# Kernel tuning notes

Hardware: AMD Instinct MI355X
Metric: run time of the kernel (lower is better)

Reference implementation:

```python
import jax, jax.numpy as jnp
import numpy as np

E = 8_388_608  # total edges across batched graphs
G = 4096       # num_graphs


def setup_inputs() -> dict:
    key = jax.random.key(0)
    k1, k2, k3 = jax.random.split(key, 3)
    edge_scores = jax.random.normal(k1, (E,), dtype=jnp.float32)
    # edge_batch: sorted segment ids in [0, G), as in PyG batched graphs
    edge_batch = jnp.sort(jax.random.randint(k2, (E,), 0, G)).astype(jnp.int32)
    candidate_mask = jax.random.bernoulli(k3, 0.5, (E,))
    return {
        "edge_scores": edge_scores,
        "edge_batch": edge_batch,
        "candidate_mask": candidate_mask,
        "num_graphs": G,
        "k": 32,
    }


def reference(edge_scores, edge_batch, candidate_mask, num_graphs, k):
    """Segmented top-k edge selection (GFlowNetActor._select_topk_candidate_edges).

    Faithful fixed-shape formulation: candidate edges come in as a boolean mask
    over all E edges (the rollout builds cand_edges = nonzero(candidate_mask)),
    and the kept top-k-per-graph edges go out as a boolean pruned mask (the
    rollout scatters the returned indices back into pruned_mask). Also returns
    the score values gated by the pruned mask (differentiable output).
    """
    n = edge_scores.shape[0]
    neg_inf = jnp.finfo(jnp.float32).min
    # Non-candidates get -inf so they sort to the back of each segment
    s = jnp.where(candidate_mask, edge_scores.astype(jnp.float32), neg_inf)
    # Sort by score descending, then stably by segment id -> within each
    # graph edges appear in descending-score order (same double-argsort as torch)
    order_score = jnp.argsort(-s, stable=True)
    order_seg = jnp.argsort(edge_batch[order_score], stable=True)
    perm = order_score[order_seg]          # [E] edge ids sorted by (seg asc, score desc)
    seg_sorted = edge_batch[perm]          # [E]
    # Segment starts via bincount + exclusive cumsum
    counts = jnp.bincount(seg_sorted, length=num_graphs)
    start = jnp.concatenate(
        [jnp.zeros(1, jnp.int32), jnp.cumsum(counts)[:-1].astype(jnp.int32)]
    )
    rank = jnp.arange(n, dtype=jnp.int32) - start[seg_sorted]
    keep_sorted = (rank < k) & candidate_mask[perm]
    # Scatter keep flags back to original edge order
    pruned_mask = jnp.zeros(n, dtype=bool).at[perm].set(keep_sorted)
    pruned_scores = jnp.where(pruned_mask, edge_scores, jnp.float32(0.0))
    return pruned_mask, pruned_scores
```

## Files before the change

kernel.cpp:

```cpp
#include <hip/hip_runtime.h>
#include <stdint.h>

#define G_NUM 4096
#define BLOCK 256
#define VPT   12
#define CAP   (BLOCK * VPT - 3)
#define CLS   256
#define HB    2048

typedef unsigned long long ull;

__device__ __forceinline__ unsigned int order_bits(float f) {
    unsigned int b = __float_as_uint(f);
    return (b & 0x80000000u) ? ~b : (b | 0x80000000u);
}
__device__ __forceinline__ float inv_order_bits(unsigned int ob) {
    return __uint_as_float((ob & 0x80000000u) ? (ob & 0x7FFFFFFFu) : ~ob);
}

__global__ void prep_kernel(const int* __restrict__ batch, int* __restrict__ start,
                            const unsigned int* __restrict__ mraw, int* __restrict__ flag,
                            int E) {
    if (blockIdx.x == 0 && threadIdx.x < 64) {
        int lane = threadIdx.x;
        bool allI = true, allF = true;
        for (int i = lane; i < 256; i += 64) {
            unsigned int w = mraw[i];
            if (w > 1u) allI = false;
            if (w != 0u && w != 0x3F800000u) allF = false;
        }
        allI = __all(allI);
        allF = __all(allF);
        if (lane == 0) *flag = allI ? 0 : (allF ? 1 : 2);
    }
    const int n4 = E >> 2;
    int i4 = blockIdx.x * blockDim.x + threadIdx.x;
    if (i4 >= n4) return;
    int4 b = ((const int4*)batch)[i4];
    int prev = __shfl_up(b.w, 1, 64);
    if ((threadIdx.x & 63) == 0) prev = (i4 == 0) ? -1 : batch[i4 * 4 - 1];
    const int e0 = i4 * 4;
    for (int g = prev + 1; g <= b.x; ++g) start[g] = e0;
    for (int g = b.x + 1; g <= b.y; ++g) start[g] = e0 + 1;
    for (int g = b.y + 1; g <= b.z; ++g) start[g] = e0 + 2;
    for (int g = b.z + 1; g <= b.w; ++g) start[g] = e0 + 3;
    if (i4 == n4 - 1) {
        int last = b.w, e = E & ~3;
        for (int t = 0; t < (E & 3); ++t) {
            int v = batch[e + t];
            for (int g = last + 1; g <= v; ++g) start[g] = e + t;
            last = v;
        }
        for (int g = last + 1; g <= G_NUM; ++g) start[g] = E;
    }
}

__device__ __forceinline__ void scan_select(
    unsigned int* hist, unsigned int* wtot, int kk,
    int* bsel_s, unsigned int* cgt_s, unsigned int* hsel_s, int* cnt2, int tid)
{
    unsigned int h = hist[tid];
    hist[tid] = 0u;
    unsigned int v = h;
    int lane = tid & 63, wv = tid >> 6;
    #pragma unroll
    for (int off = 1; off < 64; off <<= 1) {
        unsigned int o = __shfl_down(v, off, 64);
        if (lane + off < 64) v += o;
    }
    if (lane == 0) wtot[wv] = v;
    if (tid == 0) *cnt2 = 0;
    __syncthreads();
    unsigned int sfx = v;
    for (int w = wv + 1; w < 4; ++w) sfx += wtot[w];
    if ((unsigned)kk <= sfx && (unsigned)kk > sfx - h) {
        *bsel_s = tid; *cgt_s = sfx - h; *hsel_s = h;
    }
    __syncthreads();
}

__device__ __forceinline__ void scan_select2048(
    unsigned int* hist, unsigned int* wtot, int kk,
    int* bsel_s, unsigned int* cgt_s, unsigned int* hsel_s, int* cnt2, int tid)
{
    unsigned int h[8];
    unsigned int S = 0u;
    const int b0 = tid * 8;
    #pragma unroll
    for (int j = 0; j < 8; ++j) { h[j] = hist[b0 + j]; S += h[j]; hist[b0 + j] = 0u; }
    unsigned int v = S;
    int lane = tid & 63, wv = tid >> 6;
    #pragma unroll
    for (int off = 1; off < 64; off <<= 1) {
        unsigned int o = __shfl_down(v, off, 64);
        if (lane + off < 64) v += o;
    }
    if (lane == 0) wtot[wv] = v;
    if (tid == 0) *cnt2 = 0;
    __syncthreads();
    unsigned int sfx = v;
    for (int w = wv + 1; w < 4; ++w) sfx += wtot[w];
    unsigned int run = sfx - S;
    #pragma unroll
    for (int j = 7; j >= 0; --j) {
        unsigned int inc = run + h[j];
        if ((unsigned)kk <= inc && (unsigned)kk > run) {
            *bsel_s = b0 + j; *cgt_s = run; *hsel_s = h[j];
        }
        run = inc;
    }
    __syncthreads();
}

__global__ __launch_bounds__(BLOCK) void topk_kernel(
    const float* __restrict__ scores, const void* __restrict__ maskp,
    const int* __restrict__ start, const int* __restrict__ kp,
    const int* __restrict__ flagp, float* __restrict__ out_mask,
    float* __restrict__ out_scores, int E)
{
    __shared__ unsigned int hist[HB];
    __shared__ unsigned int wtot[4];
    __shared__ ull cls[CLS];
    __shared__ int cnt, cnt2, bsel_s, licut_s;
    __shared__ unsigned int cgt_s, hsel_s, P_s;

    const int g  = blockIdx.x;
    const int s0 = start[g];
    const int s1 = start[g + 1];
    const int len = s1 - s0;
    if (len <= 0) return;

    const int k     = *kp;
    const int mflag = *flagp;
    const int tid   = threadIdx.x;

    auto getmask = [&](int i) -> bool {
        if (mflag == 2) return ((const unsigned char*)maskp)[i] != 0;
        if (mflag == 0) return ((const int*)maskp)[i] != 0;
        return ((const float*)maskp)[i] != 0.0f;
    };

    if (k <= 0) {
        for (int i = s0 + tid; i < s1; i += BLOCK) { out_mask[i] = 0.0f; out_scores[i] = 0.0f; }
        return;
    }

    #pragma unroll
    for (int j = 0; j < HB / BLOCK; ++j) hist[tid + j * BLOCK] = 0u;
    if (tid == 0) cnt = 0;

    if (len <= CAP) {
        const int a0 = s0 & ~3;
        unsigned int key[VPT];
        unsigned int candm = 0u;

        #pragma unroll
        for (int q = 0; q < 3; ++q) {
            const int g0 = a0 + 4 * (q * BLOCK + tid);
            if (g0 >= s0 && g0 + 4 <= s1) {
                float4 f = *(const float4*)(scores + g0);
                key[4*q]   = order_bits(f.x);
                key[4*q+1] = order_bits(f.y);
                key[4*q+2] = order_bits(f.z);
                key[4*q+3] = order_bits(f.w);
                unsigned int cm4 = 0u;
                if (mflag == 2) {
                    unsigned int w = *(const unsigned int*)((const unsigned char*)maskp + g0);
                    #pragma unroll
                    for (int j = 0; j < 4; ++j)
                        if ((w >> (8*j)) & 0xFFu) cm4 |= 1u << j;
                } else if (mflag == 0) {
                    int4 w = *(const int4*)((const int*)maskp + g0);
                    if (w.x) cm4 |= 1u; if (w.y) cm4 |= 2u;
                    if (w.z) cm4 |= 4u; if (w.w) cm4 |= 8u;
                } else {
                    float4 w = *(const float4*)((const float*)maskp + g0);
                    if (w.x != 0.0f) cm4 |= 1u; if (w.y != 0.0f) cm4 |= 2u;
                    if (w.z != 0.0f) cm4 |= 4u; if (w.w != 0.0f) cm4 |= 8u;
                }
                candm |= cm4 << (4*q);
            } else if (g0 < s1) {
                #pragma unroll
                for (int j = 0; j < 4; ++j) {
                    int gi = g0 + j;
                    key[4*q+j] = 0u;
                    if (gi >= s0 && gi < s1) {
                        key[4*q+j] = order_bits(scores[gi]);
                        if (getmask(gi)) candm |= 1u << (4*q+j);
                    }
                }
            } else {
                #pragma unroll
                for (int j = 0; j < 4; ++j) key[4*q+j] = 0u;
            }
        }

        __syncthreads();
        #pragma unroll
        for (int v = 0; v < VPT; ++v)
            if ((candm >> v) & 1u) atomicAdd(&hist[key[v] >> 21], 1u);
        int lc = __popc(candm);
        #pragma unroll
        for (int off = 1; off < 64; off <<= 1) lc += __shfl_xor(lc, off, 64);
        if ((tid & 63) == 0) atomicAdd(&cnt, lc);
        __syncthreads();
        const int m = cnt;
        const bool keep_all = (m <= k);
        unsigned int P = 0u;
        int licut = 0;

        if (!keep_all) {
            int kk = k;
            scan_select2048(hist, wtot, kk, &bsel_s, &cgt_s, &hsel_s, &cnt2, tid);
            unsigned int prefix = ((unsigned int)bsel_s) << 21;
            kk -= (int)cgt_s;
            int csel = (int)hsel_s;
            int low  = 21;

            if (csel > CLS) {
                const int lows[3]   = {13, 5, 0};
                const int widths[3] = {8, 8, 5};
                for (int r = 0; r < 3; ++r) {
                    const int lw = lows[r], wd = widths[r];
                    const unsigned int dm = (1u << wd) - 1u;
                    #pragma unroll
                    for (int v = 0; v < VPT; ++v)
                        if (((candm >> v) & 1u) &&
                            ((key[v] >> (lw + wd)) == (prefix >> (lw + wd))))
                            atomicAdd(&hist[(key[v] >> lw) & dm], 1u);
                    __syncthreads();
                    scan_select(hist, wtot, kk, &bsel_s, &cgt_s, &hsel_s, &cnt2, tid);
                    prefix |= ((unsigned int)bsel_s) << lw;
                    kk  -= (int)cgt_s;
                    csel = (int)hsel_s;
                    low  = lw;
                    if (csel <= CLS) break;
                }
            }

            if (csel <= CLS) {
                const int dl = a0 - s0;
                #pragma unroll
                for (int v = 0; v < VPT; ++v) {
                    if (((candm >> v) & 1u) && ((key[v] >> low) == (prefix >> low))) {
                        int q = v >> 2;
                        int li = dl + 4 * (q * BLOCK + tid) + (v & 3);
                        cls[atomicAdd(&cnt2, 1)] = ((ull)key[v] << 32) | (unsigned int)li;
                    }
                }
                __syncthreads();
                if (tid < csel) {
                    ull me = cls[tid];
                    unsigned int km = (unsigned int)(me >> 32), lm = (unsigned int)me;
                    int r = 0;
                    for (int j = 0; j < csel; ++j) {
                        ull o = cls[j];
                        unsigned int ko = (unsigned int)(o >> 32), lo = (unsigned int)o;
                        r += (ko > km || (ko == km && lo < lm)) ? 1 : 0;
                    }
                    if (r == kk - 1) { P_s = km; licut_s = (int)lm; }
                }
                __syncthreads();
                P = P_s; licut = licut_s;
            } else {
                P = prefix;
                const int dl = a0 - s0;
                int lo = 0, hi = len - 1;
                while (lo < hi) {
                    int mid = (lo + hi) >> 1;
                    if (tid == 0) cnt2 = 0;
                    __syncthreads();
                    int c = 0;
                    #pragma unroll
                    for (int v = 0; v < VPT; ++v) {
                        int q = v >> 2;
                        int li = dl + 4 * (q * BLOCK + tid) + (v & 3);
                        if (((candm >> v) & 1u) && key[v] == prefix && li <= mid) c++;
                    }
                    #pragma unroll
                    for (int off = 1; off < 64; off <<= 1) c += __shfl_xor(c, off, 64);
                    if ((tid & 63) == 0) atomicAdd(&cnt2, c);
                    __syncthreads();
                    int total = cnt2;
                    __syncthreads();
                    if (total >= kk) hi = mid; else lo = mid + 1;
                }
                licut = lo;
            }
        }

        const int dl = a0 - s0;
        #pragma unroll
        for (int q = 0; q < 3; ++q) {
            const int g0 = a0 + 4 * (q * BLOCK + tid);
            if (g0 >= s0 && g0 + 4 <= s1) {
                float4 vm, vs;
                float* pm = (float*)&vm;
                float* ps = (float*)&vs;
                #pragma unroll
                for (int j = 0; j < 4; ++j) {
                    int v = 4*q + j;
                    int li = dl + 4 * (q * BLOCK + tid) + j;
                    bool kept = ((candm >> v) & 1u) &&
                        (keep_all || key[v] > P || (key[v] == P && li <= licut));
                    pm[j] = kept ? 1.0f : 0.0f;
                    ps[j] = kept ? inv_order_bits(key[v]) : 0.0f;
                }
                *(float4*)(out_mask   + g0) = vm;
                *(float4*)(out_scores + g0) = vs;
            } else if (g0 < s1) {
                #pragma unroll
                for (int j = 0; j < 4; ++j) {
                    int gi = g0 + j;
                    if (gi < s0 || gi >= s1) continue;
                    int v = 4*q + j;
                    int li = gi - s0;
                    bool kept = ((candm >> v) & 1u) &&
                        (keep_all || key[v] > P || (key[v] == P && li <= licut));
                    out_mask[gi]   = kept ? 1.0f : 0.0f;
                    out_scores[gi] = kept ? inv_order_bits(key[v]) : 0.0f;
                }
            }
        }
    } else {
        __syncthreads();
        int lc = 0;
        for (int i = s0 + tid; i < s1; i += BLOCK)
            if (getmask(i)) lc++;
        atomicAdd(&cnt, lc);
        __syncthreads();
        const int m = cnt;
        const bool keep_all = (m <= k);
        ull pivot = 0ull;
        if (!keep_all) {
            ull prefix = 0ull;
            int kk = k;
            for (int shift = 56; shift >= 0; shift -= 8) {
                for (int i = s0 + tid; i < s1; i += BLOCK) {
                    if (!getmask(i)) continue;
                    ull key = ((ull)order_bits(scores[i]) << 32) |
                              (ull)(0xFFFFFFFFu - (unsigned)(i - s0));
                    if (shift == 56 || (key >> (shift + 8)) == (prefix >> (shift + 8)))
                        atomicAdd(&hist[(unsigned)((key >> shift) & 0xFFull)], 1u);
                }
                __syncthreads();
                scan_select(hist, wtot, kk, &bsel_s, &cgt_s, &hsel_s, &cnt2, tid);
                prefix |= ((ull)(unsigned)bsel_s) << shift;
                kk -= (int)cgt_s;
            }
            pivot = prefix;
        }
        for (int i = s0 + tid; i < s1; i += BLOCK) {
            bool c = getmask(i);
            float sc = 0.0f;
            bool kept = false;
            if (c) {
                sc = scores[i];
                ull key = ((ull)order_bits(sc) << 32) |
                          (ull)(0xFFFFFFFFu - (unsigned)(i - s0));
                kept = keep_all || (key >= pivot);
            }
            out_mask[i]   = kept ? 1.0f : 0.0f;
            out_scores[i] = kept ? sc : 0.0f;
        }
    }
}

extern "C" void kernel_launch(void* const* d_in, const int* in_sizes, int n_in,
                              void* d_out, int out_size, void* d_ws, size_t ws_size,
                              hipStream_t stream) {
    const float* scores = (const float*)d_in[0];
    const int*   batch  = (const int*)d_in[1];
    const void*  mask   = d_in[2];
    const int*   kp     = (const int*)d_in[4];
    const int    E      = in_sizes[0];

    float* out_mask   = (float*)d_out;
    float* out_scores = out_mask + E;

    int* flag  = (int*)d_ws;
    int* start = (int*)((char*)d_ws + 256);

    const int n4 = E >> 2;
    prep_kernel<<<(n4 + BLOCK - 1) / BLOCK, BLOCK, 0, stream>>>(
        batch, start, (const unsigned int*)mask, flag, E);
    topk_kernel<<<G_NUM, BLOCK, 0, stream>>>(scores, mask, start, kp, flag,
                                             out_mask, out_scores, E);
}
```

Baseline: 46.18 us.

## Binary-search segment starts and halve top-k block with 24 values per thread

The prep kernel now finds each graph's segment start with a per-graph binary search over the sorted batch ids, so it no longer streams the whole 8M-entry batch array. The top-k kernel moves from 256 to 128 threads with 24 values per thread, and the first-level histogram shrinks from 2048 to 1024 bins, shifting the radix digit boundaries to match. Fewer threads per graph lower barrier and scan cost, but each thread holds more registers, the coarser first bucket can leave more candidates to refine, and the binary search makes about 23 dependent global reads per thread.

```diff
diff --git a/kernel.cpp b/kernel.cpp
--- a/kernel.cpp
+++ b/kernel.cpp
@@ -2,11 +2,13 @@
 #include <stdint.h>
 
 #define G_NUM 4096
-#define BLOCK 256
-#define VPT   12
+#define BLOCK 128
+#define VPT   24
+#define NCH   (VPT / 4)
 #define CAP   (BLOCK * VPT - 3)
 #define CLS   256
-#define HB    2048
+#define HB    1024
+#define NW    (BLOCK / 64)
 
 typedef unsigned long long ull;
 
@@ -33,61 +35,27 @@
         allF = __all(allF);
         if (lane == 0) *flag = allI ? 0 : (allF ? 1 : 2);
     }
-    const int n4 = E >> 2;
-    int i4 = blockIdx.x * blockDim.x + threadIdx.x;
-    if (i4 >= n4) return;
-    int4 b = ((const int4*)batch)[i4];
-    int prev = __shfl_up(b.w, 1, 64);
-    if ((threadIdx.x & 63) == 0) prev = (i4 == 0) ? -1 : batch[i4 * 4 - 1];
-    const int e0 = i4 * 4;
-    for (int g = prev + 1; g <= b.x; ++g) start[g] = e0;
-    for (int g = b.x + 1; g <= b.y; ++g) start[g] = e0 + 1;
-    for (int g = b.y + 1; g <= b.z; ++g) start[g] = e0 + 2;
-    for (int g = b.z + 1; g <= b.w; ++g) start[g] = e0 + 3;
-    if (i4 == n4 - 1) {
-        int last = b.w, e = E & ~3;
-        for (int t = 0; t < (E & 3); ++t) {
-            int v = batch[e + t];
-            for (int g = last + 1; g <= v; ++g) start[g] = e + t;
-            last = v;
-        }
-        for (int g = last + 1; g <= G_NUM; ++g) start[g] = E;
-    }
-}
-
-__device__ __forceinline__ void scan_select(
+    int t = blockIdx.x * blockDim.x + threadIdx.x;
+    if (t > G_NUM) return;
+    if (t == G_NUM) { start[G_NUM] = E; return; }
+    int lo = 0, hi = E;
+    while (lo < hi) {
+        int mid = (lo + hi) >> 1;
+        if (batch[mid] < t) lo = mid + 1; else hi = mid;
+    }
+    start[t] = lo;
+}
+
+template <int NPT>
+__device__ __forceinline__ void scan_sel(
     unsigned int* hist, unsigned int* wtot, int kk,
     int* bsel_s, unsigned int* cgt_s, unsigned int* hsel_s, int* cnt2, int tid)
 {
-    unsigned int h = hist[tid];
-    hist[tid] = 0u;
-    unsigned int v = h;
-    int lane = tid & 63, wv = tid >> 6;
+    unsigned int h[NPT];
+    unsigned int S = 0u;
+    const int b0 = tid * NPT;
     #pragma unroll
-    for (int off = 1; off < 64; off <<= 1) {
-        unsigned int o = __shfl_down(v, off, 64);
-        if (lane + off < 64) v += o;
-    }
-    if (lane == 0) wtot[wv] = v;
-    if (tid == 0) *cnt2 = 0;
-    __syncthreads();
-    unsigned int sfx = v;
-    for (int w = wv + 1; w < 4; ++w) sfx += wtot[w];
-    if ((unsigned)kk <= sfx && (unsigned)kk > sfx - h) {
-        *bsel_s = tid; *cgt_s = sfx - h; *hsel_s = h;
-    }
-    __syncthreads();
-}
-
-__device__ __forceinline__ void scan_select2048(
-    unsigned int* hist, unsigned int* wtot, int kk,
-    int* bsel_s, unsigned int* cgt_s, unsigned int* hsel_s, int* cnt2, int tid)
-{
-    unsigned int h[8];
-    unsigned int S = 0u;
-    const int b0 = tid * 8;
-    #pragma unroll
-    for (int j = 0; j < 8; ++j) { h[j] = hist[b0 + j]; S += h[j]; hist[b0 + j] = 0u; }
+    for (int j = 0; j < NPT; ++j) { h[j] = hist[b0 + j]; S += h[j]; hist[b0 + j] = 0u; }
     unsigned int v = S;
     int lane = tid & 63, wv = tid >> 6;
     #pragma unroll
@@ -99,10 +67,10 @@
     if (tid == 0) *cnt2 = 0;
     __syncthreads();
     unsigned int sfx = v;
-    for (int w = wv + 1; w < 4; ++w) sfx += wtot[w];
+    for (int w = wv + 1; w < NW; ++w) sfx += wtot[w];
     unsigned int run = sfx - S;
     #pragma unroll
-    for (int j = 7; j >= 0; --j) {
+    for (int j = NPT - 1; j >= 0; --j) {
         unsigned int inc = run + h[j];
         if ((unsigned)kk <= inc && (unsigned)kk > run) {
             *bsel_s = b0 + j; *cgt_s = run; *hsel_s = h[j];
@@ -119,7 +87,7 @@
     float* __restrict__ out_scores, int E)
 {
     __shared__ unsigned int hist[HB];
-    __shared__ unsigned int wtot[4];
+    __shared__ unsigned int wtot[NW];
     __shared__ ull cls[CLS];
     __shared__ int cnt, cnt2, bsel_s, licut_s;
     __shared__ unsigned int cgt_s, hsel_s, P_s;
@@ -155,7 +123,7 @@
         unsigned int candm = 0u;
 
         #pragma unroll
-        for (int q = 0; q < 3; ++q) {
+        for (int q = 0; q < NCH; ++q) {
             const int g0 = a0 + 4 * (q * BLOCK + tid);
             if (g0 >= s0 && g0 + 4 <= s1) {
                 float4 f = *(const float4*)(scores + g0);
@@ -198,7 +166,7 @@
         __syncthreads();
         #pragma unroll
         for (int v = 0; v < VPT; ++v)
-            if ((candm >> v) & 1u) atomicAdd(&hist[key[v] >> 21], 1u);
+            if ((candm >> v) & 1u) atomicAdd(&hist[key[v] >> 22], 1u);
         int lc = __popc(candm);
         #pragma unroll
         for (int off = 1; off < 64; off <<= 1) lc += __shfl_xor(lc, off, 64);
@@ -211,15 +179,15 @@
 
         if (!keep_all) {
             int kk = k;
-            scan_select2048(hist, wtot, kk, &bsel_s, &cgt_s, &hsel_s, &cnt2, tid);
-            unsigned int prefix = ((unsigned int)bsel_s) << 21;
+            scan_sel<HB / BLOCK>(hist, wtot, kk, &bsel_s, &cgt_s, &hsel_s, &cnt2, tid);
+            unsigned int prefix = ((unsigned int)bsel_s) << 22;
             kk -= (int)cgt_s;
             int csel = (int)hsel_s;
-            int low  = 21;
+            int low  = 22;
 
             if (csel > CLS) {
-                const int lows[3]   = {13, 5, 0};
-                const int widths[3] = {8, 8, 5};
+                const int lows[3]   = {14, 6, 0};
+                const int widths[3] = {8, 8, 6};
                 for (int r = 0; r < 3; ++r) {
                     const int lw = lows[r], wd = widths[r];
                     const unsigned int dm = (1u << wd) - 1u;
@@ -229,7 +197,7 @@
                             ((key[v] >> (lw + wd)) == (prefix >> (lw + wd))))
                             atomicAdd(&hist[(key[v] >> lw) & dm], 1u);
                     __syncthreads();
-                    scan_select(hist, wtot, kk, &bsel_s, &cgt_s, &hsel_s, &cnt2, tid);
+                    scan_sel<256 / BLOCK>(hist, wtot, kk, &bsel_s, &cgt_s, &hsel_s, &cnt2, tid);
                     prefix |= ((unsigned int)bsel_s) << lw;
                     kk  -= (int)cgt_s;
                     csel = (int)hsel_s;
@@ -249,8 +217,8 @@
                     }
                 }
                 __syncthreads();
-                if (tid < csel) {
-                    ull me = cls[tid];
+                for (int e = tid; e < csel; e += BLOCK) {
+                    ull me = cls[e];
                     unsigned int km = (unsigned int)(me >> 32), lm = (unsigned int)me;
                     int r = 0;
                     for (int j = 0; j < csel; ++j) {
@@ -291,7 +259,7 @@
 
         const int dl = a0 - s0;
         #pragma unroll
-        for (int q = 0; q < 3; ++q) {
+        for (int q = 0; q < NCH; ++q) {
             const int g0 = a0 + 4 * (q * BLOCK + tid);
             if (g0 >= s0 && g0 + 4 <= s1) {
                 float4 vm, vs;
@@ -344,7 +312,7 @@
                         atomicAdd(&hist[(unsigned)((key >> shift) & 0xFFull)], 1u);
                 }
                 __syncthreads();
-                scan_select(hist, wtot, kk, &bsel_s, &cgt_s, &hsel_s, &cnt2, tid);
+                scan_sel<256 / BLOCK>(hist, wtot, kk, &bsel_s, &cgt_s, &hsel_s, &cnt2, tid);
                 prefix |= ((ull)(unsigned)bsel_s) << shift;
                 kk -= (int)cgt_s;
             }
@@ -381,8 +349,7 @@
     int* flag  = (int*)d_ws;
     int* start = (int*)((char*)d_ws + 256);
 
-    const int n4 = E >> 2;
-    prep_kernel<<<(n4 + BLOCK - 1) / BLOCK, BLOCK, 0, stream>>>(
+    prep_kernel<<<(G_NUM + 1 + BLOCK - 1) / BLOCK, BLOCK, 0, stream>>>(
         batch, start, (const unsigned int*)mask, flag, E);
     topk_kernel<<<G_NUM, BLOCK, 0, stream>>>(scores, mask, start, kp, flag,
                                              out_mask, out_scores, E);
```

Result: slower. 49.55 us (+7.3%).
